# Kernel optimization log

Hardware: AMD Instinct MI355X
Metric: run time of the kernel (lower is better)

The kernel has to match this reference:

```python
import jax, jax.numpy as jnp
import numpy as np

T, D_MODEL, NH, DH, NE, TOPK, DHID = 8192, 1024, 8, 128, 8, 2, 512

def setup_inputs() -> dict:
    key = jax.random.key(0)
    ks = jax.random.split(key, 6)
    s = 0.02
    return {
        'x': jax.random.normal(ks[0], (T, D_MODEL), jnp.float32),
        'in_w': jax.random.normal(ks[1], (NH * DH, D_MODEL), jnp.float32) * s,
        'in_b': jnp.zeros((NH * DH,), jnp.float32),
        'router_w': jax.random.normal(ks[2], (NH, NE, DH), jnp.float32) * s,
        'w_in': jax.random.normal(ks[3], (NH, NE, DHID, DH), jnp.float32) * s,
        'w_out': jax.random.normal(ks[4], (NH, NE, DHID, DH), jnp.float32) * s,
        'out_w': jax.random.normal(ks[5], (D_MODEL, NH * DH), jnp.float32) * s,
        'out_b': jnp.zeros((D_MODEL,), jnp.float32),
    }

def reference(x, in_w, in_b, router_w, w_in, w_out, out_w, out_b):
    # Project to latent heads: (T, Nh, dh)
    h = (x @ in_w.T + in_b).reshape(T, NH, DH)
    # Router logits in fp32 (router_fp32=True, no bias, no jitter)
    logits = jnp.einsum('tnd,ned->tne', h.astype(jnp.float32), router_w.astype(jnp.float32))
    vals, idx = jax.lax.top_k(logits, TOPK)            # (T, Nh, k)
    w = jax.nn.softmax(vals, axis=-1).astype(h.dtype)   # (T, Nh, k)
    # Combine top-k weights into a dense per-expert gate (T, Nh, Ne)
    gate = jnp.sum(jax.nn.one_hot(idx, NE, dtype=h.dtype) * w[..., None], axis=2)
    # Expert FFN: y = gelu(x W_in^T) W_out  (exact erf gelu as torch F.gelu)
    hid = jax.nn.gelu(jnp.einsum('tnd,nefd->tnef', h, w_in), approximate=False)  # (T,Nh,Ne,DHID)
    ye = jnp.einsum('tnef,nefd->tned', hid, w_out)       # (T, Nh, Ne, dh)
    y = jnp.einsum('tne,tned->tnd', gate, ye)            # weighted scatter-combine
    # Output projection back to d_model
    return y.reshape(T, NH * DH) @ out_w.T + out_b
```

## Files before the change

### kernel.cpp

```cpp
#include <hip/hip_runtime.h>
#include <hip/hip_bf16.h>
#include <cmath>

#define T_TOK 8192
#define DMODEL 1024
#define NHEAD 8
#define DH 128
#define NEXP 8
#define NNE 64
#define DHID 512

typedef __bf16 bf16x8 __attribute__((ext_vector_type(8)));
typedef float f32x4 __attribute__((ext_vector_type(4)));
typedef unsigned short u16x8 __attribute__((ext_vector_type(8)));

#define GLDS16(g, l) __builtin_amdgcn_global_load_lds( \
    (const __attribute__((address_space(1))) unsigned int*)(g), \
    (__attribute__((address_space(3))) unsigned int*)(l), 16, 0, 0)

static __device__ inline unsigned short f2bf(float f) {
  return __builtin_bit_cast(unsigned short, __float2bfloat16(f));
}
static __device__ inline float bf2f(unsigned short u) {
  unsigned int v = ((unsigned int)u) << 16;
  return __builtin_bit_cast(float, v);
}

static __device__ inline float gelu_f(float v) {
  const float u = v * 0.70710678118654752f;
  const float s = fabsf(u);
  const float t = __builtin_amdgcn_rcpf(fmaf(0.3275911f, s, 1.0f));
  const float e = __expf(-s * s);
  float p = fmaf(1.061405429f, t, -1.453152027f);
  p = fmaf(p, t, 1.421413741f);
  p = fmaf(p, t, -0.284496736f);
  p = fmaf(p, t, 0.254829592f);
  p = p * t;
  const float erfs = fmaf(-p, e, 1.0f);
  const float erfv = copysignf(erfs, u);
  return 0.5f * v * (1.0f + erfv);
}

__global__ __launch_bounds__(256) void prep_kernel(
    const float* __restrict__ x, const float* __restrict__ in_w,
    const float* __restrict__ out_w, const float* __restrict__ w_in,
    const float* __restrict__ wout_src, const float* __restrict__ in_b,
    const float* __restrict__ router_w,
    unsigned short* __restrict__ x_bf, unsigned short* __restrict__ inw_bf,
    unsigned short* __restrict__ outw_bf, unsigned short* __restrict__ win_bf,
    unsigned short* __restrict__ woutT, double* __restrict__ Rtp, double* __restrict__ lb)
{
  __shared__ __align__(16) char smem[17408];
  const int bid = blockIdx.x;
  const int tid = threadIdx.x;

  if (bid < NNE) {
    float (*ws)[DH+4] = (float(*)[DH+4])smem;
    const int ne = bid;
    const float* src = wout_src + (size_t)ne*DHID*DH;
    unsigned short* dst = woutT + (size_t)ne*DH*DHID;
    for (int fc = 0; fc < DHID; fc += 32) {
      __syncthreads();
      for (int i = tid; i < 32*DH; i += 256) {
        const int f = i >> 7, d = i & 127;
        ws[f][d] = src[(size_t)(fc+f)*DH + d];
      }
      __syncthreads();
      for (int i = tid; i < 32*DH; i += 256) {
        const int d = i >> 5, f = i & 31;
        dst[(size_t)d*DHID + fc + f] = f2bf(ws[f][d]);
      }
    }
  } else if (bid < NNE + 32) {
    double (*rw)[DH] = (double(*)[DH])smem;
    const int rbid = bid - NNE;
    const int n  = rbid >> 2;
    const int w  = tid >> 6;
    const int lane = tid & 63;
    const int js = ((rbid & 3) << 2) + w;
    const int j = js*64 + lane;
    for (int i = tid; i < 8*DH; i += 256)
      rw[i >> 7][i & 127] = (double)router_w[(size_t)(n*8 + (i >> 7))*DH + (i & 127)];
    __syncthreads();
    double acc[8];
    #pragma unroll
    for (int e = 0; e < 8; ++e) acc[e] = 0.0;
    const float* wp = in_w + (size_t)(n*DH)*DMODEL + j;
    #pragma unroll 8
    for (int d = 0; d < DH; ++d) {
      const double wv = (double)wp[(size_t)d*DMODEL];
      #pragma unroll
      for (int e = 0; e < 8; ++e) acc[e] += wv * rw[e][d];
    }
    #pragma unroll
    for (int e = 0; e < 8; ++e)
      Rtp[(size_t)(j >> 1)*128 + (n*8 + e)*2 + (j & 1)] = acc[e];
    if (js == 0 && lane < 8) {
      double a = 0.0;
      for (int d = 0; d < DH; ++d) a += (double)in_b[n*DH + d] * rw[lane][d];
      lb[n*8 + lane] = a;
    }
  } else {
    const int N0 = T_TOK*DMODEL/8;
    const int N1 = N0 + DMODEL*DMODEL/8;
    const int N2 = N1 + DMODEL*DMODEL/8;
    const int N3 = N2 + NNE*DHID*DH/8;
    const int nblk = 992 - 96;
    for (int i = (bid - 96)*256 + tid; i < N3; i += nblk*256) {
      const float* s; unsigned short* d; int o;
      if (i < N0)      { s = x;     d = x_bf;    o = i; }
      else if (i < N1) { s = in_w;  d = inw_bf;  o = i - N0; }
      else if (i < N2) { s = out_w; d = outw_bf; o = i - N1; }
      else             { s = w_in;  d = win_bf;  o = i - N2; }
      const float4 a = *((const float4*)s + (size_t)o*2);
      const float4 b = *((const float4*)s + (size_t)o*2 + 1);
      u16x8 v;
      v[0]=f2bf(a.x); v[1]=f2bf(a.y); v[2]=f2bf(a.z); v[3]=f2bf(a.w);
      v[4]=f2bf(b.x); v[5]=f2bf(b.y); v[6]=f2bf(b.z); v[7]=f2bf(b.w);
      *((u16x8*)d + o) = v;
    }
  }
}

__global__ __launch_bounds__(64) void router_partial(
    const float* __restrict__ x, const double* __restrict__ Rtp,
    double* __restrict__ part)
{
  const int bid = blockIdx.x;
  const int s  = bid & 3;
  const int tg = bid >> 2;
  const int t0 = tg << 3;
  const int k0 = s << 8;
  const int lane = threadIdx.x;

  double acc[8];
  #pragma unroll
  for (int t = 0; t < 8; ++t) acc[t] = 0.0;

  const float*  xb = x + (size_t)t0*DMODEL + k0;
  const double* rb = Rtp + (size_t)(k0 >> 1)*128 + lane*2;

  #pragma unroll 2
  for (int kc = 0; kc < 256; kc += 8) {
    const double* r = rb + (size_t)(kc >> 1)*128;
    const double2 r0 = *(const double2*)(r);
    const double2 r1 = *(const double2*)(r + 128);
    const double2 r2 = *(const double2*)(r + 256);
    const double2 r3 = *(const double2*)(r + 384);
    #pragma unroll
    for (int t = 0; t < 8; ++t) {
      const float4 xa = *(const float4*)(xb + (size_t)t*DMODEL + kc);
      const float4 xc = *(const float4*)(xb + (size_t)t*DMODEL + kc + 4);
      acc[t] += (double)xa.x * r0.x;
      acc[t] += (double)xa.y * r0.y;
      acc[t] += (double)xa.z * r1.x;
      acc[t] += (double)xa.w * r1.y;
      acc[t] += (double)xc.x * r2.x;
      acc[t] += (double)xc.y * r2.y;
      acc[t] += (double)xc.z * r3.x;
      acc[t] += (double)xc.w * r3.y;
    }
  }
  #pragma unroll
  for (int t = 0; t < 8; ++t)
    part[((size_t)s*T_TOK + t0 + t)*NNE + lane] = acc[t];
}

__global__ __launch_bounds__(256) void gemm1_top2(
    const unsigned short* __restrict__ A, const unsigned short* __restrict__ B,
    const float* __restrict__ bias, unsigned short* __restrict__ C,
    const double* __restrict__ part, const double* __restrict__ lb,
    int* __restrict__ counts, int* __restrict__ lists, float* __restrict__ wbuf)
{
  const int bid = blockIdx.x;
  const int t = threadIdx.x;

  if (bid < 512) {
    const int N = DMODEL, K = DMODEL;
    __shared__ __align__(16) unsigned short As[128*64];
    __shared__ __align__(16) unsigned short Bs[128*64];
    const int lane = t & 63, w = t >> 6;
    const int bm = (bid & 63) << 7, bn = (bid >> 6) << 7;
    const int wm = (w & 1) << 6, wn = (w >> 1) << 6;
    f32x4 acc[4][4];
    #pragma unroll
    for (int i = 0; i < 4; ++i)
      #pragma unroll
      for (int j = 0; j < 4; ++j)
        acc[i][j] = (f32x4){0.f, 0.f, 0.f, 0.f};

    const int srow = t >> 3;
    const int scol = ((t & 7) ^ (srow & 7)) << 3;
    const unsigned short* gA = A + (size_t)(bm + srow)*K + scol;
    const unsigned short* gB = B + (size_t)(bn + srow)*K + scol;
    const size_t row32 = (size_t)32*K;
    char* lA = (char*)As + t*16;
    char* lB = (char*)Bs + t*16;
    const int rlo = lane & 15;
    const int khi = (lane >> 4) << 4;

    int aRd[4][2], bRd[4][2];
    #pragma unroll
    for (int i = 0; i < 4; ++i) {
      const int ra = wm + i*16 + rlo;
      const int rb2 = wn + i*16 + rlo;
      #pragma unroll
      for (int ks = 0; ks < 2; ++ks) {
        aRd[i][ks] = ra*128 + ((ks*64 + khi) ^ ((ra & 7) << 4));
        bRd[i][ks] = rb2*128 + ((ks*64 + khi) ^ ((rb2 & 7) << 4));
      }
    }

    for (int k0 = 0; k0 < K; k0 += 64) {
      GLDS16(gA + k0,            lA);
      GLDS16(gA + row32 + k0,    lA + 4096);
      GLDS16(gA + 2*row32 + k0,  lA + 8192);
      GLDS16(gA + 3*row32 + k0,  lA + 12288);
      GLDS16(gB + k0,            lB);
      GLDS16(gB + row32 + k0,    lB + 4096);
      GLDS16(gB + 2*row32 + k0,  lB + 8192);
      GLDS16(gB + 3*row32 + k0,  lB + 12288);
      __syncthreads();
      #pragma unroll
      for (int ks = 0; ks < 2; ++ks) {
        bf16x8 av[4], bv[4];
        #pragma unroll
        for (int i = 0; i < 4; ++i) {
          av[i] = *(const bf16x8*)((const char*)As + aRd[i][ks]);
          bv[i] = *(const bf16x8*)((const char*)Bs + bRd[i][ks]);
        }
        #pragma unroll
        for (int i = 0; i < 4; ++i)
          #pragma unroll
          for (int j = 0; j < 4; ++j)
            acc[i][j] = __builtin_amdgcn_mfma_f32_16x16x32_bf16(av[i], bv[j], acc[i][j], 0, 0, 0);
      }
      __syncthreads();
    }
    const int rq = (lane >> 4) << 2;
    #pragma unroll
    for (int j = 0; j < 4; ++j) {
      const int col = bn + wn + j*16 + rlo;
      const float bb = bias[col];
      #pragma unroll
      for (int i = 0; i < 4; ++i) {
        const int row0 = bm + wm + i*16 + rq;
        #pragma unroll
        for (int r = 0; r < 4; ++r)
          C[(size_t)(row0 + r)*N + col] = f2bf(acc[i][j][r] + bb);
      }
    }
  } else {
    __shared__ int lcnt[NNE];
    __shared__ int lbase[NNE];
    const int u = (bid - 512)*256 + t;
    const int tok = u >> 3;
    const int head = u & 7;
    if (t < NNE) lcnt[t] = 0;
    __syncthreads();

    const size_t base = (size_t)tok*NNE + head*8;
    double l[NEXP];
    #pragma unroll
    for (int e = 0; e < NEXP; e += 2) {
      double2 p0 = *(const double2*)(part + base + e);
      double2 p1 = *(const double2*)(part + (size_t)T_TOK*NNE   + base + e);
      double2 p2 = *(const double2*)(part + (size_t)2*T_TOK*NNE + base + e);
      double2 p3 = *(const double2*)(part + (size_t)3*T_TOK*NNE + base + e);
      l[e]   = (((p0.x + p1.x) + p2.x) + p3.x) + lb[head*8 + e];
      l[e+1] = (((p0.y + p1.y) + p2.y) + p3.y) + lb[head*8 + e + 1];
    }
    int e1 = 0; double v1 = l[0];
    #pragma unroll
    for (int e = 1; e < NEXP; ++e) if (l[e] > v1) { v1 = l[e]; e1 = e; }
    int e2 = -1; double v2 = -1.0e300;
    #pragma unroll
    for (int e = 0; e < NEXP; ++e) if (e != e1 && l[e] > v2) { v2 = l[e]; e2 = e; }
    const double ed = exp(v2 - v1);
    const float w1 = (float)(1.0 / (1.0 + ed));
    const float w2 = (float)(ed / (1.0 + ed));
    const int b1 = head*NEXP + e1, b2 = head*NEXP + e2;

    wbuf[(size_t)(tok*NHEAD + head)*2 + 0] = w1;
    wbuf[(size_t)(tok*NHEAD + head)*2 + 1] = w2;

    const int p1i = atomicAdd(&lcnt[b1], 1);
    const int p2i = atomicAdd(&lcnt[b2], 1);
    __syncthreads();
    if (t < NNE) lbase[t] = atomicAdd(&counts[t], lcnt[t]);
    __syncthreads();
    lists[(size_t)b1*T_TOK + lbase[b1] + p1i] = tok*2;
    lists[(size_t)b2*T_TOK + lbase[b2] + p2i] = tok*2 + 1;
  }
}

__global__ __launch_bounds__(256) void gemm_out(
    const unsigned short* __restrict__ ye, const unsigned short* __restrict__ B,
    const float* __restrict__ bias, float* __restrict__ C)
{
  const int N = DMODEL, K = DMODEL;
  __shared__ __align__(16) unsigned short As[128*64];
  __shared__ __align__(16) unsigned short Bs[128*64];
  const int t = threadIdx.x;
  const int lane = t & 63, w = t >> 6;
  const int bm = blockIdx.x << 7, bn = blockIdx.y << 7;
  const int wm = (w & 1) << 6, wn = (w >> 1) << 6;
  f32x4 acc[4][4];
  #pragma unroll
  for (int i = 0; i < 4; ++i)
    #pragma unroll
    for (int j = 0; j < 4; ++j)
      acc[i][j] = (f32x4){0.f, 0.f, 0.f, 0.f};

  const int srow = t >> 3;
  const int scol = ((t & 7) ^ (srow & 7)) << 3;
  const unsigned short* gB = B + (size_t)(bn + srow)*K + scol;
  const size_t row32 = (size_t)32*K;
  char* lB = (char*)Bs + t*16;
  const int arow = t >> 1;
  const int ah   = (t & 1) << 5;
  const int rlo = lane & 15;
  const int khi = (lane >> 4) << 4;

  int aRd[4][2], bRd[4][2];
  #pragma unroll
  for (int i = 0; i < 4; ++i) {
    const int ra = wm + i*16 + rlo;
    const int rb2 = wn + i*16 + rlo;
    #pragma unroll
    for (int ks = 0; ks < 2; ++ks) {
      aRd[i][ks] = ra*128 + ((ks*64 + khi) ^ ((ra & 7) << 4));
      bRd[i][ks] = rb2*128 + ((ks*64 + khi) ^ ((rb2 & 7) << 4));
    }
  }
  int aWr[4];
  #pragma unroll
  for (int j = 0; j < 4; ++j)
    aWr[j] = arow*128 + (((ah + 8*j)*2) ^ ((arow & 7) << 4));

  for (int k0 = 0; k0 < K; k0 += 64) {
    GLDS16(gB + k0,            lB);
    GLDS16(gB + row32 + k0,    lB + 4096);
    GLDS16(gB + 2*row32 + k0,  lB + 8192);
    GLDS16(gB + 3*row32 + k0,  lB + 12288);
    {
      const int head = k0 >> 7;
      const int inHead = (k0 & 127) + ah;
      const unsigned short* r0 = ye + (((size_t)(bm + arow)*NHEAD + head)*2)*DH + inHead;
      const unsigned short* r1 = r0 + DH;
      #pragma unroll
      for (int j = 0; j < 4; ++j) {
        const u16x8 a = *(const u16x8*)(r0 + 8*j);
        const u16x8 b = *(const u16x8*)(r1 + 8*j);
        u16x8 s;
        #pragma unroll
        for (int q = 0; q < 8; ++q) s[q] = f2bf(bf2f(a[q]) + bf2f(b[q]));
        *(u16x8*)((char*)As + aWr[j]) = s;
      }
    }
    __syncthreads();
    #pragma unroll
    for (int ks = 0; ks < 2; ++ks) {
      bf16x8 av[4], bv[4];
      #pragma unroll
      for (int i = 0; i < 4; ++i) {
        av[i] = *(const bf16x8*)((const char*)As + aRd[i][ks]);
        bv[i] = *(const bf16x8*)((const char*)Bs + bRd[i][ks]);
      }
      #pragma unroll
      for (int i = 0; i < 4; ++i)
        #pragma unroll
        for (int j = 0; j < 4; ++j)
          acc[i][j] = __builtin_amdgcn_mfma_f32_16x16x32_bf16(av[i], bv[j], acc[i][j], 0, 0, 0);
    }
    __syncthreads();
  }
  const int rq = (lane >> 4) << 2;
  #pragma unroll
  for (int j = 0; j < 4; ++j) {
    const int col = bn + wn + j*16 + rlo;
    const float bb = bias[col];
    #pragma unroll
    for (int i = 0; i < 4; ++i) {
      const int row0 = bm + wm + i*16 + rq;
      #pragma unroll
      for (int r = 0; r < 4; ++r)
        C[(size_t)(row0 + r)*N + col] = acc[i][j][r] + bb;
    }
  }
}

__global__ __launch_bounds__(512, 4) void ffn_mfma_kernel(
    const unsigned short* __restrict__ h_bf, const unsigned short* __restrict__ win_bf,
    const unsigned short* __restrict__ woutT_bf, const int* __restrict__ counts,
    const int* __restrict__ lists, const float* __restrict__ wbuf,
    unsigned short* __restrict__ ye_buf)
{
  const int ne = blockIdx.x;
  const int n  = ne >> 3;
  const int cnt = counts[ne];
  const int t0 = blockIdx.y << 7;
  if (t0 >= cnt) return;
  const int nt = min(128, cnt - t0);

  __shared__ __align__(16) unsigned short lds[40960];
  char* const L = (char*)lds;

  const int t = threadIdx.x;
  const int lane = t & 63, w = t >> 6;
  const long lbase = (long)ne * T_TOK;

  #pragma unroll
  for (int s = 0; s < 4; ++s) {
    const int o = s*8192 + t*16;
    const int row = o >> 8;
    const int c = (t & 15) ^ (row & 7);
    const int trow = t0 + row;
    const int ts = lists[lbase + (trow < cnt ? trow : t0)];
    const unsigned short* g = h_bf + (size_t)(ts >> 1)*DMODEL + n*DH + c*8;
    GLDS16(g, L + 49152 + o);
  }

  const unsigned short* winB  = win_bf  + (size_t)ne*DHID*DH;
  const unsigned short* woutB = woutT_bf + (size_t)ne*DH*DHID;

  const int wm = (w & 3) << 5;
  const int wf = (w >> 2) << 5;
  const int wd = (w >> 2) << 6;
  const int rlo = lane & 15;
  const int kq  = lane >> 4;

  int aAddr[2][4];
  #pragma unroll
  for (int i = 0; i < 2; ++i) {
    const int tr = wm + i*16 + rlo;
    #pragma unroll
    for (int ks = 0; ks < 4; ++ks)
      aAddr[i][ks] = tr*256 + ((ks*64 + kq*16) ^ ((tr & 7) << 4));
  }
  int bAddr[2][4];
  #pragma unroll
  for (int j = 0; j < 2; ++j) {
    const int fr = wf + j*16 + rlo;
    #pragma unroll
    for (int ks = 0; ks < 4; ++ks)
      bAddr[j][ks] = fr*256 + ((ks*64 + kq*16) ^ ((fr & 7) << 4));
  }
  int hWAddr[2][2];
  #pragma unroll
  for (int j = 0; j < 2; ++j)
    #pragma unroll
    for (int i = 0; i < 2; ++i) {
      const int tcol = wm + i*16 + rlo;
      const int fb   = wf + j*16 + kq*4;
      hWAddr[j][i] = tcol*128 + ((fb*2) ^ ((tcol & 7) << 4));
    }
  int a2Addr[2][2];
  #pragma unroll
  for (int i = 0; i < 2; ++i) {
    const int tr = wm + i*16 + rlo;
    #pragma unroll
    for (int ks = 0; ks < 2; ++ks)
      a2Addr[i][ks] = tr*128 + ((ks*64 + kq*16) ^ ((tr & 7) << 4));
  }
  int b2Addr[4][2];
  #pragma unroll
  for (int j = 0; j < 4; ++j) {
    const int dr = wd + j*16 + rlo;
    #pragma unroll
    for (int ks = 0; ks < 2; ++ks)
      b2Addr[j][ks] = dr*128 + ((ks*64 + kq*16) ^ ((dr & 7) << 4));
  }

  auto stage_win = [&](int fc, int pb) {
    #pragma unroll
    for (int s = 0; s < 2; ++s) {
      const int o = s*8192 + t*16;
      const int row = o >> 8;
      const int c = (t & 15) ^ (row & 7);
      GLDS16(winB + (size_t)(fc + row)*DH + c*8, L + 16384 + pb + o);
    }
  };
  auto stage_wout = [&](int fc, int pb) {
    #pragma unroll
    for (int s = 0; s < 2; ++s) {
      const int o = s*8192 + t*16;
      const int row = o >> 7;
      const int c = (t & 7) ^ (row & 7);
      GLDS16(woutB + (size_t)row*DHID + fc + c*8, L + 32768 + pb + o);
    }
  };

  f32x4 acc2[4][2];
  #pragma unroll
  for (int j = 0; j < 4; ++j)
    #pragma unroll
    for (int i = 0; i < 2; ++i)
      acc2[j][i] = (f32x4){0.f, 0.f, 0.f, 0.f};

  stage_win(0, 0);
  stage_wout(0, 0);
  __syncthreads();
  bf16x8 aReg[2][4];
  #pragma unroll
  for (int i = 0; i < 2; ++i)
    #pragma unroll
    for (int ks = 0; ks < 4; ++ks)
      aReg[i][ks] = *(const bf16x8*)(L + 49152 + aAddr[i][ks]);
  __syncthreads();

  #pragma unroll 1
  for (int c = 0; c < DHID/64; ++c) {
    const int fc = c << 6;
    const int pb = (c & 1) << 15;
    if (c + 1 < DHID/64) {
      const int qb = pb ^ 32768;
      stage_win(fc + 64, qb);
      stage_wout(fc + 64, qb);
    }
    f32x4 acc1[2][2];
    #pragma unroll
    for (int j = 0; j < 2; ++j)
      #pragma unroll
      for (int i = 0; i < 2; ++i)
        acc1[j][i] = (f32x4){0.f,0.f,0.f,0.f};
    __builtin_amdgcn_s_setprio(1);
    #pragma unroll
    for (int ks = 0; ks < 4; ++ks) {
      bf16x8 b[2];
      #pragma unroll
      for (int j = 0; j < 2; ++j)
        b[j] = *(const bf16x8*)(L + 16384 + pb + bAddr[j][ks]);
      #pragma unroll
      for (int j = 0; j < 2; ++j)
        #pragma unroll
        for (int i = 0; i < 2; ++i)
          acc1[j][i] = __builtin_amdgcn_mfma_f32_16x16x32_bf16(b[j], aReg[i][ks], acc1[j][i], 0, 0, 0);
    }
    __builtin_amdgcn_s_setprio(0);
    #pragma unroll
    for (int j = 0; j < 2; ++j)
      #pragma unroll
      for (int i = 0; i < 2; ++i) {
        const float g0 = gelu_f(acc1[j][i][0]);
        const float g1 = gelu_f(acc1[j][i][1]);
        const float g2 = gelu_f(acc1[j][i][2]);
        const float g3 = gelu_f(acc1[j][i][3]);
        const unsigned int lo = (unsigned int)f2bf(g0) | ((unsigned int)f2bf(g1) << 16);
        const unsigned int hi = (unsigned int)f2bf(g2) | ((unsigned int)f2bf(g3) << 16);
        *(uint2*)(L + hWAddr[j][i]) = make_uint2(lo, hi);
      }
    __syncthreads();

    __builtin_amdgcn_s_setprio(1);
    #pragma unroll
    for (int ks = 0; ks < 2; ++ks) {
      bf16x8 a[2], b[4];
      #pragma unroll
      for (int i = 0; i < 2; ++i)
        a[i] = *(const bf16x8*)(L + a2Addr[i][ks]);
      #pragma unroll
      for (int j = 0; j < 4; ++j)
        b[j] = *(const bf16x8*)(L + 32768 + pb + b2Addr[j][ks]);
      #pragma unroll
      for (int j = 0; j < 4; ++j)
        #pragma unroll
        for (int i = 0; i < 2; ++i)
          acc2[j][i] = __builtin_amdgcn_mfma_f32_16x16x32_bf16(b[j], a[i], acc2[j][i], 0, 0, 0);
    }
    __builtin_amdgcn_s_setprio(0);
    __syncthreads();
  }

  #pragma unroll
  for (int i = 0; i < 2; ++i) {
    const int tr = wm + i*16 + rlo;
    if (tr < nt) {
      const int ts = lists[lbase + t0 + tr];
      const float gw = wbuf[(size_t)(ts >> 1)*NHEAD*2 + n*2 + (ts & 1)];
      unsigned short* dst = ye_buf +
          ((((size_t)(ts >> 1))*NHEAD + n)*2 + (ts & 1))*DH + wd + kq*4;
      #pragma unroll
      for (int j = 0; j < 4; ++j) {
        const unsigned int lo = (unsigned int)f2bf(gw*acc2[j][i][0]) |
                                ((unsigned int)f2bf(gw*acc2[j][i][1]) << 16);
        const unsigned int hi = (unsigned int)f2bf(gw*acc2[j][i][2]) |
                                ((unsigned int)f2bf(gw*acc2[j][i][3]) << 16);
        *(uint2*)(dst + j*16) = make_uint2(lo, hi);
      }
    }
  }
}

extern "C" void kernel_launch(void* const* d_in, const int* in_sizes, int n_in,
                              void* d_out, int out_size, void* d_ws, size_t ws_size,
                              hipStream_t stream) {
  const float* x        = (const float*)d_in[0];
  const float* in_w     = (const float*)d_in[1];
  const float* in_b     = (const float*)d_in[2];
  const float* router_w = (const float*)d_in[3];
  const float* w_in     = (const float*)d_in[4];
  const float* w_out    = (const float*)d_in[5];
  const float* out_w    = (const float*)d_in[6];
  const float* out_b    = (const float*)d_in[7];
  float* out = (float*)d_out;

  size_t off = 0;
  char* base = (char*)d_ws;
  auto alloc = [&](size_t bytes) -> void* {
    void* p = base + off;
    off += (bytes + 255) & ~(size_t)255;
    return p;
  };
  unsigned short* h_bf    = (unsigned short*)alloc((size_t)T_TOK*DMODEL*2);
  unsigned short* x_bf    = (unsigned short*)alloc((size_t)T_TOK*DMODEL*2);
  unsigned short* inw_bf  = (unsigned short*)alloc((size_t)DMODEL*DMODEL*2);
  unsigned short* outw_bf = (unsigned short*)alloc((size_t)DMODEL*DMODEL*2);
  unsigned short* win_bf  = (unsigned short*)alloc((size_t)NNE*DHID*DH*2);
  unsigned short* woutT_bf= (unsigned short*)alloc((size_t)NNE*DH*DHID*2);
  unsigned short* ye_buf  = (unsigned short*)alloc((size_t)T_TOK*NHEAD*2*DH*2);
  float*  wbuf   = (float*) alloc((size_t)T_TOK*NHEAD*2*4);
  double* Rtp    = (double*)alloc((size_t)DMODEL*NNE*8);
  double* lb     = (double*)alloc(NNE*8);
  int*    counts = (int*)   alloc(NNE*4);
  int*    lists  = (int*)   alloc((size_t)NNE*T_TOK*4);
  double* part   = (double*)ye_buf;

  hipMemsetAsync(counts, 0, NNE*4, stream);

  prep_kernel<<<992, 256, 0, stream>>>(x, in_w, out_w, w_in, w_out, in_b, router_w,
                                       x_bf, inw_bf, outw_bf, win_bf,
                                       woutT_bf, Rtp, lb);

  router_partial<<<4096, 64, 0, stream>>>(x, Rtp, part);

  gemm1_top2<<<768, 256, 0, stream>>>(x_bf, inw_bf, in_b, h_bf,
                                      part, lb, counts, lists, wbuf);

  ffn_mfma_kernel<<<dim3(NNE, T_TOK/128), 512, 0, stream>>>(
      h_bf, win_bf, woutT_bf, counts, lists, wbuf, ye_buf);

  gemm_out<<<dim3(T_TOK/128, DMODEL/128), 256, 0, stream>>>(
      ye_buf, outw_bf, out_b, out);
}
```

Before: 219.6 us.

## Split router-weight fold into its own kernel and overlap router partials with conversions

Moves the fp64 computation of the folded router matrix into a small separate kernel, which also zeroes the expert counts and so removes the memset. The router partial-logit work is merged into the conversion/transpose kernel as extra blocks, four waves per block instead of one-wave blocks. Router partials now run concurrently with the bf16 conversions and transposes rather than in a separate launch afterward. The cost is an extra small serial kernel of only 32 blocks, and the fp64 router blocks share the GPU with the bandwidth-bound conversion blocks.

```diff
diff --git a/kernel.cpp b/kernel.cpp
--- a/kernel.cpp
+++ b/kernel.cpp
@@ -41,21 +41,57 @@
   return 0.5f * v * (1.0f + erfv);
 }
 
-__global__ __launch_bounds__(256) void prep_kernel(
+__global__ __launch_bounds__(256) void reff_kernel(
+    const float* __restrict__ in_w, const float* __restrict__ in_b,
+    const float* __restrict__ router_w, double* __restrict__ Rtp,
+    double* __restrict__ lb, int* __restrict__ counts)
+{
+  __shared__ double rw[8][DH];
+  const int rbid = blockIdx.x;
+  const int tid = threadIdx.x;
+  if (rbid == 0 && tid < NNE) counts[tid] = 0;
+  const int n  = rbid >> 2;
+  const int w  = tid >> 6;
+  const int lane = tid & 63;
+  const int js = ((rbid & 3) << 2) + w;
+  const int j = js*64 + lane;
+  for (int i = tid; i < 8*DH; i += 256)
+    rw[i >> 7][i & 127] = (double)router_w[(size_t)(n*8 + (i >> 7))*DH + (i & 127)];
+  __syncthreads();
+  double acc[8];
+  #pragma unroll
+  for (int e = 0; e < 8; ++e) acc[e] = 0.0;
+  const float* wp = in_w + (size_t)(n*DH)*DMODEL + j;
+  #pragma unroll 8
+  for (int d = 0; d < DH; ++d) {
+    const double wv = (double)wp[(size_t)d*DMODEL];
+    #pragma unroll
+    for (int e = 0; e < 8; ++e) acc[e] += wv * rw[e][d];
+  }
+  #pragma unroll
+  for (int e = 0; e < 8; ++e)
+    Rtp[(size_t)(j >> 1)*128 + (n*8 + e)*2 + (j & 1)] = acc[e];
+  if (js == 0 && lane < 8) {
+    double a = 0.0;
+    for (int d = 0; d < DH; ++d) a += (double)in_b[n*DH + d] * rw[lane][d];
+    lb[n*8 + lane] = a;
+  }
+}
+
+__global__ __launch_bounds__(256) void prep_router_kernel(
     const float* __restrict__ x, const float* __restrict__ in_w,
     const float* __restrict__ out_w, const float* __restrict__ w_in,
-    const float* __restrict__ wout_src, const float* __restrict__ in_b,
-    const float* __restrict__ router_w,
+    const float* __restrict__ wout_src,
     unsigned short* __restrict__ x_bf, unsigned short* __restrict__ inw_bf,
     unsigned short* __restrict__ outw_bf, unsigned short* __restrict__ win_bf,
-    unsigned short* __restrict__ woutT, double* __restrict__ Rtp, double* __restrict__ lb)
+    unsigned short* __restrict__ woutT,
+    const double* __restrict__ Rtp, double* __restrict__ part)
 {
-  __shared__ __align__(16) char smem[17408];
+  __shared__ __align__(16) float ws[32][DH+4];
   const int bid = blockIdx.x;
   const int tid = threadIdx.x;
 
   if (bid < NNE) {
-    float (*ws)[DH+4] = (float(*)[DH+4])smem;
     const int ne = bid;
     const float* src = wout_src + (size_t)ne*DHID*DH;
     unsigned short* dst = woutT + (size_t)ne*DH*DHID;
@@ -71,42 +107,13 @@
         dst[(size_t)d*DHID + fc + f] = f2bf(ws[f][d]);
       }
     }
-  } else if (bid < NNE + 32) {
-    double (*rw)[DH] = (double(*)[DH])smem;
-    const int rbid = bid - NNE;
-    const int n  = rbid >> 2;
-    const int w  = tid >> 6;
-    const int lane = tid & 63;
-    const int js = ((rbid & 3) << 2) + w;
-    const int j = js*64 + lane;
-    for (int i = tid; i < 8*DH; i += 256)
-      rw[i >> 7][i & 127] = (double)router_w[(size_t)(n*8 + (i >> 7))*DH + (i & 127)];
-    __syncthreads();
-    double acc[8];
-    #pragma unroll
-    for (int e = 0; e < 8; ++e) acc[e] = 0.0;
-    const float* wp = in_w + (size_t)(n*DH)*DMODEL + j;
-    #pragma unroll 8
-    for (int d = 0; d < DH; ++d) {
-      const double wv = (double)wp[(size_t)d*DMODEL];
-      #pragma unroll
-      for (int e = 0; e < 8; ++e) acc[e] += wv * rw[e][d];
-    }
-    #pragma unroll
-    for (int e = 0; e < 8; ++e)
-      Rtp[(size_t)(j >> 1)*128 + (n*8 + e)*2 + (j & 1)] = acc[e];
-    if (js == 0 && lane < 8) {
-      double a = 0.0;
-      for (int d = 0; d < DH; ++d) a += (double)in_b[n*DH + d] * rw[lane][d];
-      lb[n*8 + lane] = a;
-    }
-  } else {
+  } else if (bid < 960) {
     const int N0 = T_TOK*DMODEL/8;
     const int N1 = N0 + DMODEL*DMODEL/8;
     const int N2 = N1 + DMODEL*DMODEL/8;
     const int N3 = N2 + NNE*DHID*DH/8;
-    const int nblk = 992 - 96;
-    for (int i = (bid - 96)*256 + tid; i < N3; i += nblk*256) {
+    const int nblk = 960 - 64;
+    for (int i = (bid - 64)*256 + tid; i < N3; i += nblk*256) {
       const float* s; unsigned short* d; int o;
       if (i < N0)      { s = x;     d = x_bf;    o = i; }
       else if (i < N1) { s = in_w;  d = inw_bf;  o = i - N0; }
@@ -119,51 +126,46 @@
       v[4]=f2bf(b.x); v[5]=f2bf(b.y); v[6]=f2bf(b.z); v[7]=f2bf(b.w);
       *((u16x8*)d + o) = v;
     }
-  }
-}
-
-__global__ __launch_bounds__(64) void router_partial(
-    const float* __restrict__ x, const double* __restrict__ Rtp,
-    double* __restrict__ part)
-{
-  const int bid = blockIdx.x;
-  const int s  = bid & 3;
-  const int tg = bid >> 2;
-  const int t0 = tg << 3;
-  const int k0 = s << 8;
-  const int lane = threadIdx.x;
-
-  double acc[8];
-  #pragma unroll
-  for (int t = 0; t < 8; ++t) acc[t] = 0.0;
-
-  const float*  xb = x + (size_t)t0*DMODEL + k0;
-  const double* rb = Rtp + (size_t)(k0 >> 1)*128 + lane*2;
-
-  #pragma unroll 2
-  for (int kc = 0; kc < 256; kc += 8) {
-    const double* r = rb + (size_t)(kc >> 1)*128;
-    const double2 r0 = *(const double2*)(r);
-    const double2 r1 = *(const double2*)(r + 128);
-    const double2 r2 = *(const double2*)(r + 256);
-    const double2 r3 = *(const double2*)(r + 384);
-    #pragma unroll
-    for (int t = 0; t < 8; ++t) {
-      const float4 xa = *(const float4*)(xb + (size_t)t*DMODEL + kc);
-      const float4 xc = *(const float4*)(xb + (size_t)t*DMODEL + kc + 4);
-      acc[t] += (double)xa.x * r0.x;
-      acc[t] += (double)xa.y * r0.y;
-      acc[t] += (double)xa.z * r1.x;
-      acc[t] += (double)xa.w * r1.y;
-      acc[t] += (double)xc.x * r2.x;
-      acc[t] += (double)xc.y * r2.y;
-      acc[t] += (double)xc.z * r3.x;
-      acc[t] += (double)xc.w * r3.y;
-    }
-  }
-  #pragma unroll
-  for (int t = 0; t < 8; ++t)
-    part[((size_t)s*T_TOK + t0 + t)*NNE + lane] = acc[t];
+  } else {
+    const int wid = (bid - 960)*4 + (tid >> 6);
+    const int s  = wid & 3;
+    const int tg = wid >> 2;
+    const int t0 = tg << 3;
+    const int k0 = s << 8;
+    const int lane = tid & 63;
+
+    double acc[8];
+    #pragma unroll
+    for (int t = 0; t < 8; ++t) acc[t] = 0.0;
+
+    const float*  xb = x + (size_t)t0*DMODEL + k0;
+    const double* rb = Rtp + (size_t)(k0 >> 1)*128 + lane*2;
+
+    #pragma unroll 2
+    for (int kc = 0; kc < 256; kc += 8) {
+      const double* r = rb + (size_t)(kc >> 1)*128;
+      const double2 r0 = *(const double2*)(r);
+      const double2 r1 = *(const double2*)(r + 128);
+      const double2 r2 = *(const double2*)(r + 256);
+      const double2 r3 = *(const double2*)(r + 384);
+      #pragma unroll
+      for (int t = 0; t < 8; ++t) {
+        const float4 xa = *(const float4*)(xb + (size_t)t*DMODEL + kc);
+        const float4 xc = *(const float4*)(xb + (size_t)t*DMODEL + kc + 4);
+        acc[t] += (double)xa.x * r0.x;
+        acc[t] += (double)xa.y * r0.y;
+        acc[t] += (double)xa.z * r1.x;
+        acc[t] += (double)xa.w * r1.y;
+        acc[t] += (double)xc.x * r2.x;
+        acc[t] += (double)xc.y * r2.y;
+        acc[t] += (double)xc.z * r3.x;
+        acc[t] += (double)xc.w * r3.y;
+      }
+    }
+    #pragma unroll
+    for (int t = 0; t < 8; ++t)
+      part[((size_t)s*T_TOK + t0 + t)*NNE + lane] = acc[t];
+  }
 }
 
 __global__ __launch_bounds__(256) void gemm1_top2(
@@ -626,13 +628,11 @@
   int*    lists  = (int*)   alloc((size_t)NNE*T_TOK*4);
   double* part   = (double*)ye_buf;
 
-  hipMemsetAsync(counts, 0, NNE*4, stream);
-
-  prep_kernel<<<992, 256, 0, stream>>>(x, in_w, out_w, w_in, w_out, in_b, router_w,
-                                       x_bf, inw_bf, outw_bf, win_bf,
-                                       woutT_bf, Rtp, lb);
-
-  router_partial<<<4096, 64, 0, stream>>>(x, Rtp, part);
+  reff_kernel<<<32, 256, 0, stream>>>(in_w, in_b, router_w, Rtp, lb, counts);
+
+  prep_router_kernel<<<1984, 256, 0, stream>>>(x, in_w, out_w, w_in, w_out,
+                                               x_bf, inw_bf, outw_bf, win_bf,
+                                               woutT_bf, Rtp, part);
 
   gemm1_top2<<<768, 256, 0, stream>>>(x_bf, inw_bf, in_b, h_bf,
                                       part, lb, counts, lists, wbuf);
```

Measured after the change: 253.9 us. 1.16x slower.
